# Optimization experiments

Measured on AMD Instinct MI355X. Metric: run time of the kernel, lower is better.

The kernel has to match this reference:

```python
import jax, jax.numpy as jnp
import numpy as np

B, T, E, H = 8, 1024, 1024, 16
D = E // H  # head_dim = 64
MAX_OFFSET = 0.5


def setup_inputs() -> dict:
    key = jax.random.key(0)
    ks = jax.random.split(key, 12)
    s = 0.02
    return {
        "query": jax.random.normal(ks[0], (B, T, E), jnp.float32),
        "key_": jax.random.normal(ks[1], (B, T, E), jnp.float32),
        "value": jax.random.normal(ks[2], (B, T, E), jnp.float32),
        "Wq": jax.random.normal(ks[3], (E, E), jnp.float32) * s,
        "bq": jnp.zeros((E,), jnp.float32),
        "Wk": jax.random.normal(ks[4], (E, E), jnp.float32) * s,
        "bk": jnp.zeros((E,), jnp.float32),
        "Wv": jax.random.normal(ks[5], (E, E), jnp.float32) * s,
        "bv": jnp.zeros((E,), jnp.float32),
        "Wo": jax.random.normal(ks[6], (E, E), jnp.float32) * s,
        "bo": jnp.zeros((E,), jnp.float32),
        "bias_table": jax.random.normal(ks[7], (2 * T - 1, H), jnp.float32) * s,
        "offset": jax.random.normal(ks[8], (1,), jnp.float32) * 0.1,
    }


def _temporal_bias(bias_table, offset):
    # relative position index: [T, T] in [0, 2T-2]
    coords = jnp.arange(T)
    rel = (coords[:, None] - coords[None, :]) + (T - 1)
    bounded = jnp.tanh(offset) * MAX_OFFSET  # scalar (shape (1,))
    adj = jnp.clip(rel.astype(jnp.float32) + bounded, 0.0, 2.0 * T - 2.0)
    lo = jnp.floor(adj).astype(jnp.int32)
    hi = jnp.ceil(adj).astype(jnp.int32)
    w = adj - lo.astype(jnp.float32)  # [T, T]
    lo_val = bias_table[lo]  # [T, T, H]
    hi_val = bias_table[hi]  # [T, T, H]
    bias = lo_val * (1.0 - w[..., None]) + hi_val * w[..., None]
    # -> [1, H, T, T]
    return jnp.transpose(bias, (2, 0, 1))[None]


def reference(query, key_, value, Wq, bq, Wk, bk, Wv, bv, Wo, bo, bias_table, offset):
    scale = D ** -0.5
    # torch Linear: x @ W.T + b
    q = (jnp.einsum('bte,fe->btf', query, Wq) + bq).reshape(B, T, H, D).transpose(0, 2, 1, 3)
    k = (jnp.einsum('bte,fe->btf', key_, Wk) + bk).reshape(B, T, H, D).transpose(0, 2, 1, 3)
    v = (jnp.einsum('bte,fe->btf', value, Wv) + bv).reshape(B, T, H, D).transpose(0, 2, 1, 3)
    scores = jnp.einsum('bhqd,bhkd->bhqk', q, k) * scale  # [B, H, T, T]
    scores = scores + _temporal_bias(bias_table, offset)
    attn = jax.nn.softmax(scores, axis=-1)
    out = jnp.einsum('bhqk,bhkd->bhqd', attn, v)  # [B, H, T, D]
    out = out.transpose(0, 2, 1, 3).reshape(B, T, E)
    return jnp.einsum('bte,fe->btf', out, Wo) + bo
```

## Files before the change

kernel.cpp:

```cpp
#include <hip/hip_runtime.h>
#include <hip/hip_bf16.h>
#include <stdint.h>

#define B_ 8
#define T_ 1024
#define E_ 1024
#define H_ 16
#define D_ 64
#define NREL 2047

using bf16 = __hip_bfloat16;
typedef __attribute__((ext_vector_type(8))) short bhalf8;
typedef __attribute__((ext_vector_type(4))) float f32x4;

typedef __attribute__((address_space(3))) uint32_t lds32_t;
typedef const __attribute__((address_space(1))) uint32_t glb32_t;
__device__ __forceinline__ void gld_lds16(const bf16* g, bf16* l) {
  __builtin_amdgcn_global_load_lds((glb32_t*)(const void*)g, (lds32_t*)(void*)l, 16, 0, 0);
}

__global__ __launch_bounds__(256) void cvt_f32_bf16(const float* __restrict__ s,
                                                    bf16* __restrict__ d, int n) {
  const int i = (blockIdx.x * 256 + threadIdx.x) * 8;
  if (i >= n) return;
  const float4 a = *(const float4*)(s + i);
  const float4 b = *(const float4*)(s + i + 4);
  bf16 t[8];
  t[0] = __float2bfloat16(a.x); t[1] = __float2bfloat16(a.y);
  t[2] = __float2bfloat16(a.z); t[3] = __float2bfloat16(a.w);
  t[4] = __float2bfloat16(b.x); t[5] = __float2bfloat16(b.y);
  t[6] = __float2bfloat16(b.z); t[7] = __float2bfloat16(b.w);
  *(bhalf8*)(d + i) = *(const bhalf8*)t;
}

__global__ void bias_pre(const float* __restrict__ table, const float* __restrict__ offset,
                         float* __restrict__ db) {
  const int idx = blockIdx.x * 256 + threadIdx.x;
  if (idx >= NREL * H_) return;
  const int r = idx >> 4;
  const int h = idx & 15;
  const float bounded = tanhf(offset[0]) * 0.5f;
  float adj = (float)r + bounded;
  adj = fminf(fmaxf(adj, 0.f), 2046.f);
  const int lo = (int)floorf(adj);
  const int hi = (int)ceilf(adj);
  const float wgt = adj - (float)lo;
  const float v = table[lo * H_ + h] * (1.f - wgt) + table[hi * H_ + h] * wgt;
  db[h * NREL + r] = v * 1.4426950408889634f;
}

template <int SCATTER, int F32OUT>
__global__ __launch_bounds__(256) void gemm_bt(const bf16* __restrict__ A,
                                               const bf16* __restrict__ W,
                                               const float* __restrict__ bias,
                                               void* __restrict__ dst_) {
  __shared__ bf16 As[128 * 32];
  __shared__ bf16 Bs[128 * 32];
  const int tid = threadIdx.x;
  const int lane = tid & 63;
  const int w = tid >> 6;
  const int quad = lane >> 4;
  const int l15 = lane & 15;
  const int m0 = blockIdx.x * 128;
  const int n0 = blockIdx.y * 128;
  const int wm = (w >> 1) * 64;
  const int wn = (w & 1) * 64;

  const f32x4 zero4 = {0.f, 0.f, 0.f, 0.f};
  f32x4 acc[4][4];
#pragma unroll
  for (int i = 0; i < 4; ++i)
#pragma unroll
    for (int j = 0; j < 4; ++j) acc[i][j] = zero4;

  const int srow0 = w * 32 + (lane >> 2);
  const int scol = (lane & 3) * 8;
  const bf16* Ag = A + (size_t)(m0 + srow0) * E_ + scol;
  const bf16* Wg = W + (size_t)(n0 + srow0) * E_ + scol;
  bf16* As0 = As + w * 1024 + lane * 8;
  bf16* Bs0 = Bs + w * 1024 + lane * 8;

  for (int kt = 0; kt < 32; ++kt) {
    __syncthreads();
    const int kc = kt * 32;
    gld_lds16(Ag + kc, As0);
    gld_lds16(Ag + (size_t)16 * E_ + kc, As0 + 512);
    gld_lds16(Wg + kc, Bs0);
    gld_lds16(Wg + (size_t)16 * E_ + kc, Bs0 + 512);
    __syncthreads();

    bhalf8 af[4], bfr[4];
#pragma unroll
    for (int t = 0; t < 4; ++t) {
      af[t] = *(const bhalf8*)(As + (wm + t * 16 + l15) * 32 + quad * 8);
      bfr[t] = *(const bhalf8*)(Bs + (wn + t * 16 + l15) * 32 + quad * 8);
    }
#pragma unroll
    for (int mt = 0; mt < 4; ++mt)
#pragma unroll
      for (int nt = 0; nt < 4; ++nt)
        acc[mt][nt] = __builtin_amdgcn_mfma_f32_16x16x32_bf16(af[mt], bfr[nt], acc[mt][nt], 0, 0, 0);
  }

#pragma unroll
  for (int mt = 0; mt < 4; ++mt) {
#pragma unroll
    for (int nt = 0; nt < 4; ++nt) {
      const int n = n0 + wn + nt * 16 + l15;
      const float bv = bias[n];
#pragma unroll
      for (int r = 0; r < 4; ++r) {
        const int m = m0 + wm + mt * 16 + quad * 4 + r;
        const float v = acc[mt][nt][r] + bv;
        if (SCATTER) {
          const int bb = m >> 10, t = m & 1023, hh = n >> 6, d = n & 63;
          ((bf16*)dst_)[(((size_t)bb * H_ + hh) * T_ + t) * D_ + d] = __float2bfloat16(v);
        } else if (F32OUT) {
          ((float*)dst_)[(size_t)m * E_ + n] = v;
        } else {
          ((bf16*)dst_)[(size_t)m * E_ + n] = __float2bfloat16(v);
        }
      }
    }
  }
}

__device__ __forceinline__ int ps_off(int row, int colbyte) {
  return row * 128 + (colbyte ^ ((row & 7) << 4));
}

__global__ __launch_bounds__(256, 4) void attn_kernel(const bf16* __restrict__ Q,
                                                      const bf16* __restrict__ K,
                                                      const bf16* __restrict__ V,
                                                      const float* __restrict__ db,
                                                      bf16* __restrict__ xout) {
  const int tid = threadIdx.x;
  const int lane = tid & 63;
  const int w = tid >> 6;
  const int quad = lane >> 4;
  const int l15 = lane & 15;
  const int bh = blockIdx.x;
  const int h = bh & 15;
  const int b = bh >> 4;
  const int q0 = blockIdx.y * 128;

  __shared__ bf16 Vt[64][72];
  __shared__ __align__(16) bf16 Ps[4][32 * 64];
  __shared__ float dbs[1152];

  const size_t base = (size_t)bh * T_ * D_;
  const bf16* Qp = Q + base;
  const bf16* Kp = K + base;
  const bf16* Vp = V + base;
  const float* dbh = db + h * NREL;

  for (int t = tid; t < 1151; t += 256) dbs[t] = dbh[q0 + t];

  const int qw = q0 + w * 32;
  bhalf8 aq[2][2];
#pragma unroll
  for (int mt = 0; mt < 2; ++mt)
#pragma unroll
    for (int ks = 0; ks < 2; ++ks)
      aq[mt][ks] = *(const bhalf8*)(Qp + (size_t)(qw + mt * 16 + l15) * D_ + ks * 32 + quad * 8);

  const f32x4 zero4 = {0.f, 0.f, 0.f, 0.f};
  f32x4 o[2][4];
#pragma unroll
  for (int mt = 0; mt < 2; ++mt)
#pragma unroll
    for (int nt = 0; nt < 4; ++nt) o[mt][nt] = zero4;
  float mrow[2] = {-1e30f, -1e30f};
  float lrow[2] = {0.f, 0.f};

  const int vrow0 = tid >> 3;
  const int vc8 = (tid & 7) * 8;
  bhalf8 vreg[2];
  vreg[0] = *(const bhalf8*)(Vp + (size_t)vrow0 * D_ + vc8);
  vreg[1] = *(const bhalf8*)(Vp + (size_t)(vrow0 + 32) * D_ + vc8);

  char* const psw = (char*)&Ps[w][0];

  for (int it = 0; it < 16; ++it) {
    const int kb = it * 64;
    bhalf8 bk[4][2];
#pragma unroll
    for (int nt = 0; nt < 4; ++nt) {
      const bf16* kr = Kp + (size_t)(kb + nt * 16 + l15) * D_ + quad * 8;
      bk[nt][0] = *(const bhalf8*)kr;
      bk[nt][1] = *(const bhalf8*)(kr + 32);
    }

    __syncthreads();
#pragma unroll
    for (int s = 0; s < 2; ++s) {
      const int row = vrow0 + s * 32;
      const bf16* vp = (const bf16*)&vreg[s];
      const int kvp = (row + vc8) & 63;
#pragma unroll
      for (int j = 0; j < 8; ++j) Vt[vc8 + j][kvp] = vp[j];
    }
    __syncthreads();
    if (it < 15) {
      const int kb2 = kb + 64;
      vreg[0] = *(const bhalf8*)(Vp + (size_t)(kb2 + vrow0) * D_ + vc8);
      vreg[1] = *(const bhalf8*)(Vp + (size_t)(kb2 + vrow0 + 32) * D_ + vc8);
    }

    f32x4 s4[2][4];
    __builtin_amdgcn_s_setprio(1);
#pragma unroll
    for (int nt = 0; nt < 4; ++nt) {
#pragma unroll
      for (int mt = 0; mt < 2; ++mt) {
        f32x4 a = zero4;
        a = __builtin_amdgcn_mfma_f32_16x16x32_bf16(bk[nt][0], aq[mt][0], a, 0, 0, 0);
        a = __builtin_amdgcn_mfma_f32_16x16x32_bf16(bk[nt][1], aq[mt][1], a, 0, 0, 0);
        s4[mt][nt] = a;
      }
    }
    __builtin_amdgcn_s_setprio(0);

#pragma unroll
    for (int mt = 0; mt < 2; ++mt) {
      const int ib = w * 32 + mt * 16 + l15 + 1023 - kb;
      float mnt[4];
#pragma unroll
      for (int nt = 0; nt < 4; ++nt) {
#pragma unroll
        for (int r = 0; r < 4; ++r) {
          const float sv = s4[mt][nt][r] * 0.18033688011112042f + dbs[ib - nt * 16 - quad * 4 - r];
          s4[mt][nt][r] = sv;
        }
        mnt[nt] = fmaxf(fmaxf(s4[mt][nt][0], s4[mt][nt][1]),
                        fmaxf(s4[mt][nt][2], s4[mt][nt][3]));
      }
      float tmx = fmaxf(fmaxf(mnt[0], mnt[1]), fmaxf(mnt[2], mnt[3]));
      tmx = fmaxf(tmx, __shfl_xor(tmx, 16, 64));
      tmx = fmaxf(tmx, __shfl_xor(tmx, 32, 64));
      if (!__all(tmx - mrow[mt] <= 11.0f)) {
        const float mnew = fmaxf(mrow[mt], tmx);
        const float alpha = __builtin_amdgcn_exp2f(mrow[mt] - mnew);
        mrow[mt] = mnew;
        lrow[mt] *= alpha;
#pragma unroll
        for (int nt = 0; nt < 4; ++nt) o[mt][nt] *= alpha;
      }
      const float mcur = mrow[mt];
      float psum[4];
#pragma unroll
      for (int nt = 0; nt < 4; ++nt) {
        float p0 = __builtin_amdgcn_exp2f(s4[mt][nt][0] - mcur);
        float p1 = __builtin_amdgcn_exp2f(s4[mt][nt][1] - mcur);
        float p2 = __builtin_amdgcn_exp2f(s4[mt][nt][2] - mcur);
        float p3 = __builtin_amdgcn_exp2f(s4[mt][nt][3] - mcur);
        s4[mt][nt][0] = p0; s4[mt][nt][1] = p1;
        s4[mt][nt][2] = p2; s4[mt][nt][3] = p3;
        psum[nt] = (p0 + p1) + (p2 + p3);
      }
      float sum = (psum[0] + psum[1]) + (psum[2] + psum[3]);
      sum += __shfl_xor(sum, 16, 64);
      sum += __shfl_xor(sum, 32, 64);
      lrow[mt] += sum;

#pragma unroll
      for (int nt = 0; nt < 4; ++nt) {
        alignas(8) bf16 t4[4];
#pragma unroll
        for (int r = 0; r < 4; ++r) t4[r] = __float2bfloat16(s4[mt][nt][r]);
        *(uint2*)(psw + ps_off(mt * 16 + l15, nt * 32 + quad * 8)) = *(const uint2*)t4;
      }
    }

    bhalf8 pb[2][2];
#pragma unroll
    for (int mt = 0; mt < 2; ++mt)
#pragma unroll
      for (int ks = 0; ks < 2; ++ks)
        pb[mt][ks] = *(const bhalf8*)(psw + ps_off(mt * 16 + l15, ks * 64 + quad * 16));
    const int rot = (l15 >> 3);
    __builtin_amdgcn_s_setprio(1);
#pragma unroll
    for (int nt = 0; nt < 4; ++nt) {
      const int drow = nt * 16 + l15;
#pragma unroll
      for (int ks = 0; ks < 2; ++ks) {
        const int gp = (4 * ks + quad + 2 * nt + rot) & 7;
        const bhalf8 vb = *(const bhalf8*)&Vt[drow][gp * 8];
#pragma unroll
        for (int mt = 0; mt < 2; ++mt)
          o[mt][nt] = __builtin_amdgcn_mfma_f32_16x16x32_bf16(vb, pb[mt][ks], o[mt][nt], 0, 0, 0);
      }
    }
    __builtin_amdgcn_s_setprio(0);
  }

#pragma unroll
  for (int mt = 0; mt < 2; ++mt) {
    const float inv = 1.f / lrow[mt];
#pragma unroll
    for (int nt = 0; nt < 4; ++nt) {
      alignas(8) bf16 t4[4];
#pragma unroll
      for (int r = 0; r < 4; ++r) t4[r] = __float2bfloat16(o[mt][nt][r] * inv);
      *(uint2*)(psw + ps_off(mt * 16 + l15, nt * 32 + quad * 8)) = *(const uint2*)t4;
    }
  }
#pragma unroll
  for (int t = 0; t < 4; ++t) {
    const int idx = t * 64 + lane;
    const int row = idx >> 3;
    const int c = idx & 7;
    const bhalf8 val = *(const bhalf8*)(psw + ps_off(row, c * 16));
    *(bhalf8*)&xout[((size_t)b * T_ + qw + row) * E_ + h * D_ + c * 8] = val;
  }
}

extern "C" void kernel_launch(void* const* d_in, const int* in_sizes, int n_in,
                              void* d_out, int out_size, void* d_ws, size_t ws_size,
                              hipStream_t stream) {
  const float* query = (const float*)d_in[0];
  const float* key_  = (const float*)d_in[1];
  const float* value = (const float*)d_in[2];
  const float* Wq = (const float*)d_in[3];
  const float* bq = (const float*)d_in[4];
  const float* Wk = (const float*)d_in[5];
  const float* bk = (const float*)d_in[6];
  const float* Wv = (const float*)d_in[7];
  const float* bv = (const float*)d_in[8];
  const float* Wo = (const float*)d_in[9];
  const float* bo = (const float*)d_in[10];
  const float* table = (const float*)d_in[11];
  const float* offset = (const float*)d_in[12];
  float* out = (float*)d_out;

  char* ws = (char*)d_ws;
  const size_t ME = (size_t)B_ * T_ * E_;
  const size_t EE = (size_t)E_ * E_;
  float* db = (float*)ws;
  bf16* xc  = (bf16*)(ws + 131072);
  bf16* wc  = xc + ME;
  bf16* qb  = wc + 4 * EE;
  bf16* kb  = qb + ME;
  bf16* vb2 = kb + ME;
  bf16* x2  = vb2 + ME;

  dim3 bb(256, 1, 1);
  dim3 gg(64, 8, 1);
  const int gME = (int)(ME / 8 / 256);
  const int gEE = (int)(EE / 8 / 256);

  bias_pre<<<dim3(128), bb, 0, stream>>>(table, offset, db);

  cvt_f32_bf16<<<dim3(gEE), bb, 0, stream>>>(Wq, wc + 0 * EE, (int)EE);
  cvt_f32_bf16<<<dim3(gEE), bb, 0, stream>>>(Wk, wc + 1 * EE, (int)EE);
  cvt_f32_bf16<<<dim3(gEE), bb, 0, stream>>>(Wv, wc + 2 * EE, (int)EE);
  cvt_f32_bf16<<<dim3(gEE), bb, 0, stream>>>(Wo, wc + 3 * EE, (int)EE);

  cvt_f32_bf16<<<dim3(gME), bb, 0, stream>>>(query, xc, (int)ME);
  gemm_bt<1, 0><<<gg, bb, 0, stream>>>(xc, wc + 0 * EE, bq, qb);
  cvt_f32_bf16<<<dim3(gME), bb, 0, stream>>>(key_, xc, (int)ME);
  gemm_bt<1, 0><<<gg, bb, 0, stream>>>(xc, wc + 1 * EE, bk, kb);
  cvt_f32_bf16<<<dim3(gME), bb, 0, stream>>>(value, xc, (int)ME);
  gemm_bt<1, 0><<<gg, bb, 0, stream>>>(xc, wc + 2 * EE, bv, vb2);

  attn_kernel<<<dim3(128, 8, 1), bb, 0, stream>>>(qb, kb, vb2, db, x2);

  gemm_bt<0, 1><<<gg, bb, 0, stream>>>(x2, wc + 3 * EE, bo, out);
}
```

Measured before the change: 363.0 us.

## Double-buffer V tile in attention and shrink GEMM N-tile to 64

The attention kernel now double-buffers the transposed V tile in LDS, writing the next tile after the PV MFMAs and leaving one barrier per iteration instead of two. It also prefetches the next K fragments into registers midway through the QK step. Separately, the projection GEMM uses 128x64 tiles on a doubled grid to raise occupancy and block count. The cost is more LDS and register pressure in attention, and lower arithmetic intensity per block in the GEMM.

```diff
diff --git a/kernel.cpp b/kernel.cpp
--- a/kernel.cpp
+++ b/kernel.cpp
@@ -55,30 +55,31 @@
                                                const float* __restrict__ bias,
                                                void* __restrict__ dst_) {
   __shared__ bf16 As[128 * 32];
-  __shared__ bf16 Bs[128 * 32];
+  __shared__ bf16 Bs[64 * 32];
   const int tid = threadIdx.x;
   const int lane = tid & 63;
   const int w = tid >> 6;
   const int quad = lane >> 4;
   const int l15 = lane & 15;
   const int m0 = blockIdx.x * 128;
-  const int n0 = blockIdx.y * 128;
+  const int n0 = blockIdx.y * 64;
   const int wm = (w >> 1) * 64;
-  const int wn = (w & 1) * 64;
+  const int wn = (w & 1) * 32;
 
   const f32x4 zero4 = {0.f, 0.f, 0.f, 0.f};
-  f32x4 acc[4][4];
+  f32x4 acc[4][2];
 #pragma unroll
   for (int i = 0; i < 4; ++i)
 #pragma unroll
-    for (int j = 0; j < 4; ++j) acc[i][j] = zero4;
-
-  const int srow0 = w * 32 + (lane >> 2);
+    for (int j = 0; j < 2; ++j) acc[i][j] = zero4;
+
   const int scol = (lane & 3) * 8;
-  const bf16* Ag = A + (size_t)(m0 + srow0) * E_ + scol;
-  const bf16* Wg = W + (size_t)(n0 + srow0) * E_ + scol;
+  const int srowA = w * 32 + (lane >> 2);
+  const bf16* Ag = A + (size_t)(m0 + srowA) * E_ + scol;
   bf16* As0 = As + w * 1024 + lane * 8;
-  bf16* Bs0 = Bs + w * 1024 + lane * 8;
+  const int srowB = w * 16 + (lane >> 2);
+  const bf16* Wg = W + (size_t)(n0 + srowB) * E_ + scol;
+  bf16* Bs0 = Bs + w * 512 + lane * 8;
 
   for (int kt = 0; kt < 32; ++kt) {
     __syncthreads();
@@ -86,26 +87,26 @@
     gld_lds16(Ag + kc, As0);
     gld_lds16(Ag + (size_t)16 * E_ + kc, As0 + 512);
     gld_lds16(Wg + kc, Bs0);
-    gld_lds16(Wg + (size_t)16 * E_ + kc, Bs0 + 512);
     __syncthreads();
 
-    bhalf8 af[4], bfr[4];
-#pragma unroll
-    for (int t = 0; t < 4; ++t) {
+    bhalf8 af[4], bfr[2];
+#pragma unroll
+    for (int t = 0; t < 4; ++t)
       af[t] = *(const bhalf8*)(As + (wm + t * 16 + l15) * 32 + quad * 8);
+#pragma unroll
+    for (int t = 0; t < 2; ++t)
       bfr[t] = *(const bhalf8*)(Bs + (wn + t * 16 + l15) * 32 + quad * 8);
-    }
 #pragma unroll
     for (int mt = 0; mt < 4; ++mt)
 #pragma unroll
-      for (int nt = 0; nt < 4; ++nt)
+      for (int nt = 0; nt < 2; ++nt)
         acc[mt][nt] = __builtin_amdgcn_mfma_f32_16x16x32_bf16(af[mt], bfr[nt], acc[mt][nt], 0, 0, 0);
   }
 
 #pragma unroll
   for (int mt = 0; mt < 4; ++mt) {
 #pragma unroll
-    for (int nt = 0; nt < 4; ++nt) {
+    for (int nt = 0; nt < 2; ++nt) {
       const int n = n0 + wn + nt * 16 + l15;
       const float bv = bias[n];
 #pragma unroll
@@ -144,7 +145,7 @@
   const int b = bh >> 4;
   const int q0 = blockIdx.y * 128;
 
-  __shared__ bf16 Vt[64][72];
+  __shared__ bf16 Vt[2][64][72];
   __shared__ __align__(16) bf16 Ps[4][32 * 64];
   __shared__ float dbs[1152];
 
@@ -179,61 +180,65 @@
   vreg[0] = *(const bhalf8*)(Vp + (size_t)vrow0 * D_ + vc8);
   vreg[1] = *(const bhalf8*)(Vp + (size_t)(vrow0 + 32) * D_ + vc8);
 
+#pragma unroll
+  for (int s = 0; s < 2; ++s) {
+    const int row = vrow0 + s * 32;
+    const bf16* vp = (const bf16*)&vreg[s];
+    const int kvp = (row + vc8) & 63;
+#pragma unroll
+    for (int j = 0; j < 8; ++j) Vt[0][vc8 + j][kvp] = vp[j];
+  }
+  bhalf8 bk[4][2];
+#pragma unroll
+  for (int nt = 0; nt < 4; ++nt) {
+    const bf16* kr = Kp + (size_t)(nt * 16 + l15) * D_ + quad * 8;
+    bk[nt][0] = *(const bhalf8*)kr;
+    bk[nt][1] = *(const bhalf8*)(kr + 32);
+  }
+  __syncthreads();
+  vreg[0] = *(const bhalf8*)(Vp + (size_t)(64 + vrow0) * D_ + vc8);
+  vreg[1] = *(const bhalf8*)(Vp + (size_t)(64 + vrow0 + 32) * D_ + vc8);
+
   char* const psw = (char*)&Ps[w][0];
+  const int rot = (l15 >> 3);
 
   for (int it = 0; it < 16; ++it) {
     const int kb = it * 64;
-    bhalf8 bk[4][2];
-#pragma unroll
-    for (int nt = 0; nt < 4; ++nt) {
-      const bf16* kr = Kp + (size_t)(kb + nt * 16 + l15) * D_ + quad * 8;
-      bk[nt][0] = *(const bhalf8*)kr;
-      bk[nt][1] = *(const bhalf8*)(kr + 32);
-    }
-
-    __syncthreads();
-#pragma unroll
-    for (int s = 0; s < 2; ++s) {
-      const int row = vrow0 + s * 32;
-      const bf16* vp = (const bf16*)&vreg[s];
-      const int kvp = (row + vc8) & 63;
-#pragma unroll
-      for (int j = 0; j < 8; ++j) Vt[vc8 + j][kvp] = vp[j];
-    }
-    __syncthreads();
-    if (it < 15) {
-      const int kb2 = kb + 64;
-      vreg[0] = *(const bhalf8*)(Vp + (size_t)(kb2 + vrow0) * D_ + vc8);
-      vreg[1] = *(const bhalf8*)(Vp + (size_t)(kb2 + vrow0 + 32) * D_ + vc8);
-    }
-
-    f32x4 s4[2][4];
-    __builtin_amdgcn_s_setprio(1);
-#pragma unroll
-    for (int nt = 0; nt < 4; ++nt) {
-#pragma unroll
-      for (int mt = 0; mt < 2; ++mt) {
+    const int cur = it & 1;
+
+#pragma unroll
+    for (int mt = 0; mt < 2; ++mt) {
+      f32x4 s4[4];
+      __builtin_amdgcn_s_setprio(1);
+#pragma unroll
+      for (int nt = 0; nt < 4; ++nt) {
         f32x4 a = zero4;
         a = __builtin_amdgcn_mfma_f32_16x16x32_bf16(bk[nt][0], aq[mt][0], a, 0, 0, 0);
         a = __builtin_amdgcn_mfma_f32_16x16x32_bf16(bk[nt][1], aq[mt][1], a, 0, 0, 0);
-        s4[mt][nt] = a;
-      }
-    }
-    __builtin_amdgcn_s_setprio(0);
-
-#pragma unroll
-    for (int mt = 0; mt < 2; ++mt) {
+        s4[nt] = a;
+      }
+      __builtin_amdgcn_s_setprio(0);
+
+      if (mt == 1 && it < 15) {
+        const int kb2 = kb + 64;
+#pragma unroll
+        for (int nt = 0; nt < 4; ++nt) {
+          const bf16* kr = Kp + (size_t)(kb2 + nt * 16 + l15) * D_ + quad * 8;
+          bk[nt][0] = *(const bhalf8*)kr;
+          bk[nt][1] = *(const bhalf8*)(kr + 32);
+        }
+      }
+
       const int ib = w * 32 + mt * 16 + l15 + 1023 - kb;
       float mnt[4];
 #pragma unroll
       for (int nt = 0; nt < 4; ++nt) {
 #pragma unroll
         for (int r = 0; r < 4; ++r) {
-          const float sv = s4[mt][nt][r] * 0.18033688011112042f + dbs[ib - nt * 16 - quad * 4 - r];
-          s4[mt][nt][r] = sv;
+          const float sv = s4[nt][r] * 0.18033688011112042f + dbs[ib - nt * 16 - quad * 4 - r];
+          s4[nt][r] = sv;
         }
-        mnt[nt] = fmaxf(fmaxf(s4[mt][nt][0], s4[mt][nt][1]),
-                        fmaxf(s4[mt][nt][2], s4[mt][nt][3]));
+        mnt[nt] = fmaxf(fmaxf(s4[nt][0], s4[nt][1]), fmaxf(s4[nt][2], s4[nt][3]));
       }
       float tmx = fmaxf(fmaxf(mnt[0], mnt[1]), fmaxf(mnt[2], mnt[3]));
       tmx = fmaxf(tmx, __shfl_xor(tmx, 16, 64));
@@ -250,12 +255,12 @@
       float psum[4];
 #pragma unroll
       for (int nt = 0; nt < 4; ++nt) {
-        float p0 = __builtin_amdgcn_exp2f(s4[mt][nt][0] - mcur);
-        float p1 = __builtin_amdgcn_exp2f(s4[mt][nt][1] - mcur);
-        float p2 = __builtin_amdgcn_exp2f(s4[mt][nt][2] - mcur);
-        float p3 = __builtin_amdgcn_exp2f(s4[mt][nt][3] - mcur);
-        s4[mt][nt][0] = p0; s4[mt][nt][1] = p1;
-        s4[mt][nt][2] = p2; s4[mt][nt][3] = p3;
+        float p0 = __builtin_amdgcn_exp2f(s4[nt][0] - mcur);
+        float p1 = __builtin_amdgcn_exp2f(s4[nt][1] - mcur);
+        float p2 = __builtin_amdgcn_exp2f(s4[nt][2] - mcur);
+        float p3 = __builtin_amdgcn_exp2f(s4[nt][3] - mcur);
+        s4[nt][0] = p0; s4[nt][1] = p1;
+        s4[nt][2] = p2; s4[nt][3] = p3;
         psum[nt] = (p0 + p1) + (p2 + p3);
       }
       float sum = (psum[0] + psum[1]) + (psum[2] + psum[3]);
@@ -267,7 +272,7 @@
       for (int nt = 0; nt < 4; ++nt) {
         alignas(8) bf16 t4[4];
 #pragma unroll
-        for (int r = 0; r < 4; ++r) t4[r] = __float2bfloat16(s4[mt][nt][r]);
+        for (int r = 0; r < 4; ++r) t4[r] = __float2bfloat16(s4[nt][r]);
         *(uint2*)(psw + ps_off(mt * 16 + l15, nt * 32 + quad * 8)) = *(const uint2*)t4;
       }
     }
@@ -278,7 +283,6 @@
 #pragma unroll
       for (int ks = 0; ks < 2; ++ks)
         pb[mt][ks] = *(const bhalf8*)(psw + ps_off(mt * 16 + l15, ks * 64 + quad * 16));
-    const int rot = (l15 >> 3);
     __builtin_amdgcn_s_setprio(1);
 #pragma unroll
     for (int nt = 0; nt < 4; ++nt) {
@@ -286,13 +290,30 @@
 #pragma unroll
       for (int ks = 0; ks < 2; ++ks) {
         const int gp = (4 * ks + quad + 2 * nt + rot) & 7;
-        const bhalf8 vb = *(const bhalf8*)&Vt[drow][gp * 8];
+        const bhalf8 vb = *(const bhalf8*)&Vt[cur][drow][gp * 8];
 #pragma unroll
         for (int mt = 0; mt < 2; ++mt)
           o[mt][nt] = __builtin_amdgcn_mfma_f32_16x16x32_bf16(vb, pb[mt][ks], o[mt][nt], 0, 0, 0);
       }
     }
     __builtin_amdgcn_s_setprio(0);
+
+    if (it < 15) {
+#pragma unroll
+      for (int s = 0; s < 2; ++s) {
+        const int row = vrow0 + s * 32;
+        const bf16* vp = (const bf16*)&vreg[s];
+        const int kvp = (row + vc8) & 63;
+#pragma unroll
+        for (int j = 0; j < 8; ++j) Vt[cur ^ 1][vc8 + j][kvp] = vp[j];
+      }
+      if (it < 14) {
+        const int kb2 = kb + 128;
+        vreg[0] = *(const bhalf8*)(Vp + (size_t)(kb2 + vrow0) * D_ + vc8);
+        vreg[1] = *(const bhalf8*)(Vp + (size_t)(kb2 + vrow0 + 32) * D_ + vc8);
+      }
+    }
+    __syncthreads();
   }
 
 #pragma unroll
@@ -346,7 +367,7 @@
   bf16* x2  = vb2 + ME;
 
   dim3 bb(256, 1, 1);
-  dim3 gg(64, 8, 1);
+  dim3 gg(64, 16, 1);
   const int gME = (int)(ME / 8 / 256);
   const int gEE = (int)(EE / 8 / 256);
 
```

Measured after the change: 408.0 us. 12.4% more time.

## Fuse fp32-to-bf16 input conversion into a single batched QKV projection GEMM

Applied to the files above, without the earlier changes.

Replaces three separate activation conversion kernels and three projection GEMMs with one gemm_qkv launch over a z-dimension of 3. The kernel loads fp32 activations directly, converts them to bf16 in registers while prefetching the next K tile, and writes them to LDS. This removes the bf16 staging buffer round trip and five kernel launches, and gives one larger grid. In exchange, each block reads twice the A bytes per tile through plain global loads instead of async LDS loads.

```diff
diff --git a/kernel.cpp b/kernel.cpp
--- a/kernel.cpp
+++ b/kernel.cpp
@@ -47,6 +47,106 @@
   const float wgt = adj - (float)lo;
   const float v = table[lo * H_ + h] * (1.f - wgt) + table[hi * H_ + h] * wgt;
   db[h * NREL + r] = v * 1.4426950408889634f;
+}
+
+__global__ __launch_bounds__(256, 3) void gemm_qkv(const float* __restrict__ Xq,
+                                                   const float* __restrict__ Xk,
+                                                   const float* __restrict__ Xv,
+                                                   const bf16* __restrict__ Wc,
+                                                   const float* __restrict__ bqp,
+                                                   const float* __restrict__ bkp,
+                                                   const float* __restrict__ bvp,
+                                                   bf16* __restrict__ dst) {
+  __shared__ bf16 As[128 * 32];
+  __shared__ bf16 Bs[128 * 32];
+  const int tid = threadIdx.x;
+  const int lane = tid & 63;
+  const int w = tid >> 6;
+  const int quad = lane >> 4;
+  const int l15 = lane & 15;
+  const int m0 = blockIdx.x * 128;
+  const int n0 = blockIdx.y * 128;
+  const int z = blockIdx.z;
+  const float* A = (z == 0) ? Xq : ((z == 1) ? Xk : Xv);
+  const float* bias = (z == 0) ? bqp : ((z == 1) ? bkp : bvp);
+  const bf16* W = Wc + (size_t)z * E_ * E_;
+  bf16* out = dst + (size_t)z * B_ * T_ * D_ * H_;
+  const int wm = (w >> 1) * 64;
+  const int wn = (w & 1) * 64;
+
+  const f32x4 zero4 = {0.f, 0.f, 0.f, 0.f};
+  f32x4 acc[4][4];
+#pragma unroll
+  for (int i = 0; i < 4; ++i)
+#pragma unroll
+    for (int j = 0; j < 4; ++j) acc[i][j] = zero4;
+
+  const int srow = w * 32 + (lane >> 2);
+  const int scol = (lane & 3) * 8;
+  const float* Ag = A + (size_t)(m0 + srow) * E_ + scol;
+  const bf16* Wg = W + (size_t)(n0 + srow) * E_ + scol;
+  bf16* As0 = As + w * 1024 + lane * 8;
+  bf16* Bs0 = Bs + w * 1024 + lane * 8;
+
+  float4 p0 = *(const float4*)(Ag);
+  float4 p1 = *(const float4*)(Ag + 4);
+  float4 p2 = *(const float4*)(Ag + (size_t)16 * E_);
+  float4 p3 = *(const float4*)(Ag + (size_t)16 * E_ + 4);
+
+  for (int kt = 0; kt < 32; ++kt) {
+    __syncthreads();
+    const int kc = kt * 32;
+    gld_lds16(Wg + kc, Bs0);
+    gld_lds16(Wg + (size_t)16 * E_ + kc, Bs0 + 512);
+    const float4 a0 = p0, a1 = p1, a2 = p2, a3 = p3;
+    if (kt < 31) {
+      const int kc2 = kc + 32;
+      p0 = *(const float4*)(Ag + kc2);
+      p1 = *(const float4*)(Ag + kc2 + 4);
+      p2 = *(const float4*)(Ag + (size_t)16 * E_ + kc2);
+      p3 = *(const float4*)(Ag + (size_t)16 * E_ + kc2 + 4);
+    }
+    bf16 t[8];
+    t[0] = __float2bfloat16(a0.x); t[1] = __float2bfloat16(a0.y);
+    t[2] = __float2bfloat16(a0.z); t[3] = __float2bfloat16(a0.w);
+    t[4] = __float2bfloat16(a1.x); t[5] = __float2bfloat16(a1.y);
+    t[6] = __float2bfloat16(a1.z); t[7] = __float2bfloat16(a1.w);
+    *(bhalf8*)As0 = *(const bhalf8*)t;
+    t[0] = __float2bfloat16(a2.x); t[1] = __float2bfloat16(a2.y);
+    t[2] = __float2bfloat16(a2.z); t[3] = __float2bfloat16(a2.w);
+    t[4] = __float2bfloat16(a3.x); t[5] = __float2bfloat16(a3.y);
+    t[6] = __float2bfloat16(a3.z); t[7] = __float2bfloat16(a3.w);
+    *(bhalf8*)(As0 + 512) = *(const bhalf8*)t;
+    __syncthreads();
+
+    bhalf8 af[4], bfr[4];
+#pragma unroll
+    for (int t2 = 0; t2 < 4; ++t2) {
+      af[t2] = *(const bhalf8*)(As + (wm + t2 * 16 + l15) * 32 + quad * 8);
+      bfr[t2] = *(const bhalf8*)(Bs + (wn + t2 * 16 + l15) * 32 + quad * 8);
+    }
+#pragma unroll
+    for (int mt = 0; mt < 4; ++mt)
+#pragma unroll
+      for (int nt = 0; nt < 4; ++nt)
+        acc[mt][nt] = __builtin_amdgcn_mfma_f32_16x16x32_bf16(af[mt], bfr[nt], acc[mt][nt], 0, 0, 0);
+  }
+
+#pragma unroll
+  for (int mt = 0; mt < 4; ++mt) {
+#pragma unroll
+    for (int nt = 0; nt < 4; ++nt) {
+      const int n = n0 + wn + nt * 16 + l15;
+      const float bv = bias[n];
+#pragma unroll
+      for (int r = 0; r < 4; ++r) {
+        const int m = m0 + wm + mt * 16 + quad * 4 + r;
+        const float v = acc[mt][nt][r] + bv;
+        const int bb = m >> 10, tq = m & 1023, hh = n >> 6, d = n & 63;
+        out[(((size_t)bb * H_ + hh) * T_ + tq) * D_ + d] = __float2bfloat16(v);
+      }
+    }
+  }
 }
 
 template <int SCATTER, int F32OUT>
@@ -338,16 +438,13 @@
   const size_t ME = (size_t)B_ * T_ * E_;
   const size_t EE = (size_t)E_ * E_;
   float* db = (float*)ws;
-  bf16* xc  = (bf16*)(ws + 131072);
-  bf16* wc  = xc + ME;
+  bf16* wc  = (bf16*)(ws + 131072);
   bf16* qb  = wc + 4 * EE;
   bf16* kb  = qb + ME;
   bf16* vb2 = kb + ME;
   bf16* x2  = vb2 + ME;
 
   dim3 bb(256, 1, 1);
-  dim3 gg(64, 8, 1);
-  const int gME = (int)(ME / 8 / 256);
   const int gEE = (int)(EE / 8 / 256);
 
   bias_pre<<<dim3(128), bb, 0, stream>>>(table, offset, db);
@@ -357,14 +454,9 @@
   cvt_f32_bf16<<<dim3(gEE), bb, 0, stream>>>(Wv, wc + 2 * EE, (int)EE);
   cvt_f32_bf16<<<dim3(gEE), bb, 0, stream>>>(Wo, wc + 3 * EE, (int)EE);
 
-  cvt_f32_bf16<<<dim3(gME), bb, 0, stream>>>(query, xc, (int)ME);
-  gemm_bt<1, 0><<<gg, bb, 0, stream>>>(xc, wc + 0 * EE, bq, qb);
-  cvt_f32_bf16<<<dim3(gME), bb, 0, stream>>>(key_, xc, (int)ME);
-  gemm_bt<1, 0><<<gg, bb, 0, stream>>>(xc, wc + 1 * EE, bk, kb);
-  cvt_f32_bf16<<<dim3(gME), bb, 0, stream>>>(value, xc, (int)ME);
-  gemm_bt<1, 0><<<gg, bb, 0, stream>>>(xc, wc + 2 * EE, bv, vb2);
+  gemm_qkv<<<dim3(64, 8, 3), bb, 0, stream>>>(query, key_, value, wc, bq, bk, bv, qb);
 
   attn_kernel<<<dim3(128, 8, 1), bb, 0, stream>>>(qb, kb, vb2, db, x2);
 
-  gemm_bt<0, 1><<<gg, bb, 0, stream>>>(x2, wc + 3 * EE, bo, out);
-}
+  gemm_bt<0, 1><<<dim3(64, 8, 1), bb, 0, stream>>>(x2, wc + 3 * EE, bo, out);
+}
```

New measurement: 354.8 us. 1.02x faster.
